# Kernel tuning notes

Hardware: AMD Instinct MI355X
Metric: run time of the kernel (lower is better)

## Reference

```python
import jax, jax.numpy as jnp
import numpy as np

N, C = 2097152, 32

def setup_inputs() -> dict:
    key = jax.random.key(0)
    k1, k2, k3 = jax.random.split(key, 3)
    inp = jax.random.normal(k1, (N, C), dtype=jnp.float32)
    # target: soft label distribution per row (rows sum to 1)
    t = jax.random.uniform(k2, (N, C), dtype=jnp.float32)
    target = t / jnp.sum(t, axis=-1, keepdims=True)
    weight = jax.random.uniform(k3, (C,), dtype=jnp.float32)
    return {"input": inp, "target": target, "weight": weight}

def reference(input, target, weight):
    # Algebraic fusion of the original per-class loop:
    # loss_n = sum_c target[n,c] * weight[c] * (-log_softmax(input)[n,c])
    logp = jax.nn.log_softmax(input, axis=-1)  # [N, C]
    per_row = -jnp.sum(target * weight[None, :] * logp, axis=-1)  # [N]
    return jnp.mean(per_row)  # reduction='mean'
```

## Files before the change

kernel.cpp:

```cpp
#include <hip/hip_runtime.h>

#define NCLASS 32
#define NBLOCKS 2048
#define BLOCKSZ 256
#define GPB (BLOCKSZ / 8)
#define TG (NBLOCKS * GPB)

typedef float floatx4 __attribute__((ext_vector_type(4)));

__device__ __forceinline__ float red8_sum(float x) {
    x += __int_as_float(__builtin_amdgcn_mov_dpp(__float_as_int(x), 0xB1, 0xF, 0xF, true));
    x += __int_as_float(__builtin_amdgcn_mov_dpp(__float_as_int(x), 0x4E, 0xF, 0xF, true));
    x += __int_as_float(__builtin_amdgcn_mov_dpp(__float_as_int(x), 0x141, 0xF, 0xF, true));
    return x;
}

__global__ __launch_bounds__(BLOCKSZ)
void ce_partial_kernel(const float* __restrict__ inp,
                       const float* __restrict__ tgt,
                       const float* __restrict__ wgt,
                       float* __restrict__ partial,
                       int nrows) {
    const int t = threadIdx.x;
    const int r = t & 7;
    const int g = blockIdx.x * GPB + (t >> 3);

    const floatx4 w4 = reinterpret_cast<const floatx4*>(wgt)[r];

    float accAL = 0.0f;
    float accB  = 0.0f;

    const floatx4* pin = reinterpret_cast<const floatx4*>(inp) + (size_t)g * 8 + r;
    const floatx4* ptg = reinterpret_cast<const floatx4*>(tgt) + (size_t)g * 8 + r;
    const size_t step = (size_t)TG * 8;

    int row = g;
    for (; row + 3 * TG < nrows; row += 4 * TG, pin += 4 * step, ptg += 4 * step) {
        const floatx4 x0 = __builtin_nontemporal_load(pin);
        const floatx4 x1 = __builtin_nontemporal_load(pin + step);
        const floatx4 x2 = __builtin_nontemporal_load(pin + 2 * step);
        const floatx4 x3 = __builtin_nontemporal_load(pin + 3 * step);
        const floatx4 t0 = __builtin_nontemporal_load(ptg);
        const floatx4 t1 = __builtin_nontemporal_load(ptg + step);
        const floatx4 t2 = __builtin_nontemporal_load(ptg + 2 * step);
        const floatx4 t3 = __builtin_nontemporal_load(ptg + 3 * step);

        float S0 = (__expf(x0.x) + __expf(x0.y)) + (__expf(x0.z) + __expf(x0.w));
        float S1 = (__expf(x1.x) + __expf(x1.y)) + (__expf(x1.z) + __expf(x1.w));
        float S2 = (__expf(x2.x) + __expf(x2.y)) + (__expf(x2.z) + __expf(x2.w));
        float S3 = (__expf(x3.x) + __expf(x3.y)) + (__expf(x3.z) + __expf(x3.w));

        const float a0 = t0.x * w4.x, a1 = t0.y * w4.y, a2 = t0.z * w4.z, a3 = t0.w * w4.w;
        const float b0 = t1.x * w4.x, b1 = t1.y * w4.y, b2 = t1.z * w4.z, b3 = t1.w * w4.w;
        const float c0 = t2.x * w4.x, c1 = t2.y * w4.y, c2 = t2.z * w4.z, c3 = t2.w * w4.w;
        const float d0 = t3.x * w4.x, d1 = t3.y * w4.y, d2 = t3.z * w4.z, d3 = t3.w * w4.w;

        float A0 = (a0 + a1) + (a2 + a3);
        float A1 = (b0 + b1) + (b2 + b3);
        float A2 = (c0 + c1) + (c2 + c3);
        float A3 = (d0 + d1) + (d2 + d3);

        accB += (a0 * x0.x + a1 * x0.y) + (a2 * x0.z + a3 * x0.w);
        accB += (b0 * x1.x + b1 * x1.y) + (b2 * x1.z + b3 * x1.w);
        accB += (c0 * x2.x + c1 * x2.y) + (c2 * x2.z + c3 * x2.w);
        accB += (d0 * x3.x + d1 * x3.y) + (d2 * x3.z + d3 * x3.w);

        S0 = red8_sum(S0);  A0 = red8_sum(A0);
        S1 = red8_sum(S1);  A1 = red8_sum(A1);
        S2 = red8_sum(S2);  A2 = red8_sum(A2);
        S3 = red8_sum(S3);  A3 = red8_sum(A3);

        if (r == 0) {
            accAL += A0 * __logf(S0) + A1 * __logf(S1);
            accAL += A2 * __logf(S2) + A3 * __logf(S3);
        }
    }
    for (; row < nrows; row += TG, pin += step, ptg += step) {
        const floatx4 xa = *pin;
        const floatx4 ta = *ptg;
        float Sa = (__expf(xa.x) + __expf(xa.y)) + (__expf(xa.z) + __expf(xa.w));
        const float a0 = ta.x * w4.x, a1 = ta.y * w4.y, a2 = ta.z * w4.z, a3 = ta.w * w4.w;
        float Aa = (a0 + a1) + (a2 + a3);
        accB += (a0 * xa.x + a1 * xa.y) + (a2 * xa.z + a3 * xa.w);
        Sa = red8_sum(Sa);  Aa = red8_sum(Aa);
        if (r == 0) accAL += Aa * __logf(Sa);
    }

    float v = accAL - accB;

    v += __shfl_xor(v, 1);
    v += __shfl_xor(v, 2);
    v += __shfl_xor(v, 4);
    v += __shfl_xor(v, 8);
    v += __shfl_xor(v, 16);
    v += __shfl_xor(v, 32);

    __shared__ float sacc[BLOCKSZ / 64];
    if ((t & 63) == 0) sacc[t >> 6] = v;
    __syncthreads();
    if (t == 0) {
        float s = 0.0f;
        #pragma unroll
        for (int i = 0; i < BLOCKSZ / 64; ++i) s += sacc[i];
        partial[blockIdx.x] = s;
    }
}

__global__ __launch_bounds__(BLOCKSZ)
void ce_final_kernel(const float* __restrict__ partial, int n,
                     float* __restrict__ out, float inv_n) {
    const int t = threadIdx.x;
    float s = 0.0f;
    for (int i = t; i < n; i += BLOCKSZ) s += partial[i];
    s += __shfl_xor(s, 1);
    s += __shfl_xor(s, 2);
    s += __shfl_xor(s, 4);
    s += __shfl_xor(s, 8);
    s += __shfl_xor(s, 16);
    s += __shfl_xor(s, 32);
    __shared__ float sacc[BLOCKSZ / 64];
    if ((t & 63) == 0) sacc[t >> 6] = s;
    __syncthreads();
    if (t == 0) {
        float tot = 0.0f;
        #pragma unroll
        for (int i = 0; i < BLOCKSZ / 64; ++i) tot += sacc[i];
        out[0] = tot * inv_n;
    }
}

extern "C" void kernel_launch(void* const* d_in, const int* in_sizes, int n_in,
                              void* d_out, int out_size, void* d_ws, size_t ws_size,
                              hipStream_t stream) {
    const float* inp = (const float*)d_in[0];
    const float* tgt = (const float*)d_in[1];
    const float* wgt = (const float*)d_in[2];
    float* out = (float*)d_out;
    float* partial = (float*)d_ws;

    const int nrows = in_sizes[0] / NCLASS;

    ce_partial_kernel<<<NBLOCKS, BLOCKSZ, 0, stream>>>(inp, tgt, wgt, partial, nrows);
    ce_final_kernel<<<1, BLOCKSZ, 0, stream>>>(partial, NBLOCKS, out,
                                               1.0f / (float)nrows);
}
```

Before: 101.3 us.

## Fuse final reduction into main kernel via last-block atomic counter

Replaces the separate single-block final reduction kernel with a last-block-done pattern: each block writes its partial, fences, and bumps an atomic counter, and the last block sums all partials and writes the mean. A memset of the counter is added before the launch. Nontemporal loads are also swapped for ordinary loads. The aim is to remove one kernel launch; the cost is the extra memset operation, plus any change in cache behaviour from dropping the nontemporal hints.

```diff
diff --git a/kernel.cpp b/kernel.cpp
--- a/kernel.cpp
+++ b/kernel.cpp
@@ -16,11 +16,13 @@
 }
 
 __global__ __launch_bounds__(BLOCKSZ)
-void ce_partial_kernel(const float* __restrict__ inp,
-                       const float* __restrict__ tgt,
-                       const float* __restrict__ wgt,
-                       float* __restrict__ partial,
-                       int nrows) {
+void ce_fused_kernel(const float* __restrict__ inp,
+                     const float* __restrict__ tgt,
+                     const float* __restrict__ wgt,
+                     float* __restrict__ partial,
+                     unsigned int* __restrict__ counter,
+                     float* __restrict__ out,
+                     int nrows, float inv_n) {
     const int t = threadIdx.x;
     const int r = t & 7;
     const int g = blockIdx.x * GPB + (t >> 3);
@@ -36,14 +38,14 @@
 
     int row = g;
     for (; row + 3 * TG < nrows; row += 4 * TG, pin += 4 * step, ptg += 4 * step) {
-        const floatx4 x0 = __builtin_nontemporal_load(pin);
-        const floatx4 x1 = __builtin_nontemporal_load(pin + step);
-        const floatx4 x2 = __builtin_nontemporal_load(pin + 2 * step);
-        const floatx4 x3 = __builtin_nontemporal_load(pin + 3 * step);
-        const floatx4 t0 = __builtin_nontemporal_load(ptg);
-        const floatx4 t1 = __builtin_nontemporal_load(ptg + step);
-        const floatx4 t2 = __builtin_nontemporal_load(ptg + 2 * step);
-        const floatx4 t3 = __builtin_nontemporal_load(ptg + 3 * step);
+        const floatx4 x0 = pin[0];
+        const floatx4 x1 = pin[step];
+        const floatx4 x2 = pin[2 * step];
+        const floatx4 x3 = pin[3 * step];
+        const floatx4 t0 = ptg[0];
+        const floatx4 t1 = ptg[step];
+        const floatx4 t2 = ptg[2 * step];
+        const floatx4 t3 = ptg[3 * step];
 
         float S0 = (__expf(x0.x) + __expf(x0.y)) + (__expf(x0.z) + __expf(x0.w));
         float S1 = (__expf(x1.x) + __expf(x1.y)) + (__expf(x1.z) + __expf(x1.w));
@@ -96,6 +98,7 @@
     v += __shfl_xor(v, 32);
 
     __shared__ float sacc[BLOCKSZ / 64];
+    __shared__ int is_last;
     if ((t & 63) == 0) sacc[t >> 6] = v;
     __syncthreads();
     if (t == 0) {
@@ -103,29 +106,31 @@
         #pragma unroll
         for (int i = 0; i < BLOCKSZ / 64; ++i) s += sacc[i];
         partial[blockIdx.x] = s;
+        __threadfence();
+        unsigned int old = atomicAdd(counter, 1u);
+        is_last = (old == (unsigned)(gridDim.x - 1)) ? 1 : 0;
     }
-}
+    __syncthreads();
 
-__global__ __launch_bounds__(BLOCKSZ)
-void ce_final_kernel(const float* __restrict__ partial, int n,
-                     float* __restrict__ out, float inv_n) {
-    const int t = threadIdx.x;
-    float s = 0.0f;
-    for (int i = t; i < n; i += BLOCKSZ) s += partial[i];
-    s += __shfl_xor(s, 1);
-    s += __shfl_xor(s, 2);
-    s += __shfl_xor(s, 4);
-    s += __shfl_xor(s, 8);
-    s += __shfl_xor(s, 16);
-    s += __shfl_xor(s, 32);
-    __shared__ float sacc[BLOCKSZ / 64];
-    if ((t & 63) == 0) sacc[t >> 6] = s;
-    __syncthreads();
-    if (t == 0) {
-        float tot = 0.0f;
-        #pragma unroll
-        for (int i = 0; i < BLOCKSZ / 64; ++i) tot += sacc[i];
-        out[0] = tot * inv_n;
+    if (is_last) {
+        __threadfence();
+        volatile const float* vp = partial;
+        float s = 0.0f;
+        for (int i = t; i < NBLOCKS; i += BLOCKSZ) s += vp[i];
+        s += __shfl_xor(s, 1);
+        s += __shfl_xor(s, 2);
+        s += __shfl_xor(s, 4);
+        s += __shfl_xor(s, 8);
+        s += __shfl_xor(s, 16);
+        s += __shfl_xor(s, 32);
+        if ((t & 63) == 0) sacc[t >> 6] = s;
+        __syncthreads();
+        if (t == 0) {
+            float tot = 0.0f;
+            #pragma unroll
+            for (int i = 0; i < BLOCKSZ / 64; ++i) tot += sacc[i];
+            out[0] = tot * inv_n;
+        }
     }
 }
 
@@ -137,10 +142,12 @@
     const float* wgt = (const float*)d_in[2];
     float* out = (float*)d_out;
     float* partial = (float*)d_ws;
+    unsigned int* counter = (unsigned int*)((char*)d_ws + NBLOCKS * sizeof(float));
 
     const int nrows = in_sizes[0] / NCLASS;
 
-    ce_partial_kernel<<<NBLOCKS, BLOCKSZ, 0, stream>>>(inp, tgt, wgt, partial, nrows);
-    ce_final_kernel<<<1, BLOCKSZ, 0, stream>>>(partial, NBLOCKS, out,
-                                               1.0f / (float)nrows);
+    hipMemsetAsync(counter, 0, sizeof(unsigned int), stream);
+
+    ce_fused_kernel<<<NBLOCKS, BLOCKSZ, 0, stream>>>(
+        inp, tgt, wgt, partial, counter, out, nrows, 1.0f / (float)nrows);
 }
```

Result: slower. 208.3 us (+105.6%).
